# Kernel tuning notes

Hardware: AMD Instinct MI355X
Metric: run time of the kernel (lower is better)

## Reference

```python
import jax, jax.numpy as jnp
import numpy as np

NZ = 1024       # opts.nz (== NH so layer-0 input weights stack with other layers)
NH = 1024       # opts.nh
NSTATE = 64     # opts.n_state
NLAYERS = 4
MAX_PRIM_LEN = 100
T = MAX_PRIM_LEN + 1   # max_unroll=True runs exactly max_prim_len+1 steps
P_BIAS = 1.0           # opts.dec_p_bias


def setup_inputs() -> dict:
    key = jax.random.key(0)
    ks = jax.random.split(key, 9)
    s_ih = 1.0 / np.sqrt(NH)
    u = lambda k, shape: jax.random.uniform(k, shape, jnp.float32, -s_ih, s_ih)
    return {
        "z": jax.random.normal(ks[0], (1, NZ), jnp.float32),
        # torch LSTM params, gate order (i, f, g, o); layer0 input dim == NZ == NH
        "Wih": u(ks[1], (NLAYERS, 4 * NH, NH)),
        "Whh": u(ks[2], (NLAYERS, 4 * NH, NH)),
        "bih": u(ks[3], (NLAYERS, 4 * NH)),
        "bhh": u(ks[4], (NLAYERS, 4 * NH)),
        "Ws": u(ks[5], (NSTATE, NH)),
        "bs": u(ks[6], (NSTATE,)),
        "Wp": u(ks[7], (2, NH)),
        "bp": u(ks[8], (2,)),
    }


def reference(z, Wih, Whh, bih, bhh, Ws, bs, Wp, bp):
    z0 = z.reshape(-1)  # (NZ,)
    zeros = jnp.zeros_like(z0)

    def step(carry, i):
        h, c = carry                      # each (NLAYERS, NH)
        x = jnp.where(i == 0, z0, zeros)  # input is z at t=0, zeros after
        hs, cs = [], []
        inp = x
        for l in range(NLAYERS):
            gates = Wih[l] @ inp + bih[l] + Whh[l] @ h[l] + bhh[l]
            gi, gf, gg, go = jnp.split(gates, 4)
            cl = jax.nn.sigmoid(gf) * c[l] + jax.nn.sigmoid(gi) * jnp.tanh(gg)
            hl = jax.nn.sigmoid(go) * jnp.tanh(cl)
            hs.append(hl)
            cs.append(cl)
            inp = hl
        o = inp                            # top-layer output, (NH,)
        s = Ws @ o + bs                    # state head, (NSTATE,)
        logits = (Wp @ o + bp).at[0].add(P_BIAS)
        p = jax.nn.softmax(logits)         # (2,)
        last = i == T - 1                  # torch: t > max_prim_len -> force [0,1]
        p = jnp.where(last, jnp.array([0.0, 1.0], p.dtype), p)
        samp = jnp.where(last, 1, 0).astype(jnp.int64)  # max_unroll forces 0 until last
        return (jnp.stack(hs), jnp.stack(cs)), (s, p, samp)

    h0 = jnp.zeros((NLAYERS, NH), z.dtype)
    _, (states, probs, samples) = jax.lax.scan(step, (h0, h0), jnp.arange(T))
    return states[:, None, :], probs[:, None, :], samples[:, None]
```

## Files before the change

kernel.cpp:

```cpp
#include <hip/hip_runtime.h>


#define TT    101
#define NBLK  256
#define NTH   512
#define NREP  8
#define SLAB_U32 512
#define HB16_BYTES (4 * TT * NREP * SLAB_U32 * 4)
#define OUT_PROBS 6464
#define OUT_SAMP  6666
#define SENT 0xFFFFFFFFu

typedef _Float16 h2 __attribute__((ext_vector_type(2)));

__device__ __forceinline__ h2 mkh2(float a, float b) {
    h2 r; r.x = (_Float16)a; r.y = (_Float16)b; return r;
}
__device__ __forceinline__ unsigned pack2(float a, float b) {
    return __builtin_bit_cast(unsigned, mkh2(a, b));
}
__device__ __forceinline__ h2 as_h2(unsigned u) { return __builtin_bit_cast(h2, u); }

#if __has_builtin(__builtin_amdgcn_fdot2)
__device__ __forceinline__ float fdot2(h2 a, h2 b, float c) {
    return __builtin_amdgcn_fdot2(a, b, c, false);
}
#else
__device__ __forceinline__ float fdot2(h2 a, h2 b, float c) {
    return fmaf((float)a.x, (float)b.x, fmaf((float)a.y, (float)b.y, c));
}
#endif

__device__ __forceinline__ uint4 load16_bypass(const uint4* p) {
    uint4 r;
    asm volatile("global_load_dwordx4 %0, %1, off sc0 sc1\n\ts_waitcnt vmcnt(0)"
                 : "=v"(r) : "v"(p) : "memory");
    return r;
}
__device__ __forceinline__ void store4_bypass(unsigned* p, unsigned v) {
    asm volatile("global_store_dword %0, %1, off sc0 sc1" :: "v"(p), "v"(v) : "memory");
}
__device__ __forceinline__ uint4 poll16(const uint4* p) {
    uint4 r = load16_bypass(p);
    while (r.x == SENT || r.y == SENT || r.z == SENT || r.w == SENT) {
        __builtin_amdgcn_s_sleep(1);
        r = load16_bypass(p);
    }
    return r;
}

__device__ __forceinline__ float wave_sum(float x) {
    int v;
    v = __builtin_amdgcn_update_dpp(0, __builtin_bit_cast(int, x), 0x111, 0xf, 0xf, false);
    x += __builtin_bit_cast(float, v);
    v = __builtin_amdgcn_update_dpp(0, __builtin_bit_cast(int, x), 0x112, 0xf, 0xf, false);
    x += __builtin_bit_cast(float, v);
    v = __builtin_amdgcn_update_dpp(0, __builtin_bit_cast(int, x), 0x114, 0xf, 0xe, false);
    x += __builtin_bit_cast(float, v);
    v = __builtin_amdgcn_update_dpp(0, __builtin_bit_cast(int, x), 0x118, 0xf, 0xc, false);
    x += __builtin_bit_cast(float, v);
    v = __builtin_amdgcn_update_dpp(0, __builtin_bit_cast(int, x), 0x142, 0xa, 0xf, false);
    x += __builtin_bit_cast(float, v);
    v = __builtin_amdgcn_update_dpp(0, __builtin_bit_cast(int, x), 0x143, 0xc, 0xf, false);
    x += __builtin_bit_cast(float, v);
    return __builtin_bit_cast(float, __builtin_amdgcn_readlane(__builtin_bit_cast(int, x), 63));
}

__device__ __forceinline__ float sigm(float x) { return 1.f / (1.f + expf(-x)); }

__global__ __launch_bounds__(NTH, 2) void lstm_kernel(
    const float* __restrict__ z,
    const float* __restrict__ Wih, const float* __restrict__ Whh,
    const float* __restrict__ bih, const float* __restrict__ bhh,
    const float* __restrict__ Ws,  const float* __restrict__ bs,
    const float* __restrict__ Wp,  const float* __restrict__ bp,
    unsigned* __restrict__ hb16, float* __restrict__ out)
{
    const int tid  = threadIdx.x;
    const int wv   = tid >> 6;
    const int lane = tid & 63;
    const int l    = blockIdx.x >> 6;
    const int gb   = blockIdx.x & 63;
    const int uA   = (gb << 4) + (wv << 1);

    __shared__ __align__(16) uint4 vh4[256];
    __shared__ unsigned hout[8];

    h2 w[8][16];
    #pragma unroll
    for (int r = 0; r < 8; ++r) {
        const int u = uA + (r >> 2);
        const int g = r & 3;
        const size_t row = ((size_t)((l << 12) + (g << 10) + u)) << 10;
        const float4* pa = (const float4*)(Whh + row + (lane << 3));
        const float4* pb = (const float4*)(Whh + row + 512 + (lane << 3));
        const float4* pc = (const float4*)(Wih + row + (lane << 3));
        const float4* pd = (const float4*)(Wih + row + 512 + (lane << 3));
        float4 f;
        f = pa[0]; w[r][0]  = mkh2(f.x, f.y); w[r][1]  = mkh2(f.z, f.w);
        f = pa[1]; w[r][2]  = mkh2(f.x, f.y); w[r][3]  = mkh2(f.z, f.w);
        f = pb[0]; w[r][4]  = mkh2(f.x, f.y); w[r][5]  = mkh2(f.z, f.w);
        f = pb[1]; w[r][6]  = mkh2(f.x, f.y); w[r][7]  = mkh2(f.z, f.w);
        f = pc[0]; w[r][8]  = mkh2(f.x, f.y); w[r][9]  = mkh2(f.z, f.w);
        f = pc[1]; w[r][10] = mkh2(f.x, f.y); w[r][11] = mkh2(f.z, f.w);
        f = pd[0]; w[r][12] = mkh2(f.x, f.y); w[r][13] = mkh2(f.z, f.w);
        f = pd[1]; w[r][14] = mkh2(f.x, f.y); w[r][15] = mkh2(f.z, f.w);
    }

    float bA[4], bB[4];
    #pragma unroll
    for (int g = 0; g < 4; ++g) {
        const int iA = (l << 12) + (g << 10) + uA;
        bA[g] = bih[iA] + bhh[iA];
        bB[g] = bih[iA + 1] + bhh[iA + 1];
    }

    const bool role_states = (l == 0 && wv == 6);
    const bool role_probs  = (l == 1 && gb == 0 && wv == 6);
    float hw0[16], hw1[16], hb0 = 0.f, hb1 = 0.f;
    if (role_states) {
        #pragma unroll
        for (int k = 0; k < 16; ++k) hw0[k] = Ws[(gb << 10) + (lane << 4) + k];
        hb0 = bs[gb];
    } else if (role_probs) {
        #pragma unroll
        for (int k = 0; k < 16; ++k) {
            hw0[k] = Wp[(lane << 4) + k];
            hw1[k] = Wp[1024 + (lane << 4) + k];
        }
        hb0 = bp[0]; hb1 = bp[1];
    }
    int th = 0;

    float cstA = 0.f, cstB = 0.f;

    #pragma unroll 1
    for (int t = 0; t < TT; ++t) {
        const bool full = (l > 0) || (t == 0);
        const int rep = (gb + wv) & (NREP - 1);

        if (wv < 2) {
            const int c = (wv << 6) + lane;
            if (t == 0) vh4[c] = make_uint4(0, 0, 0, 0);
            else {
                const uint4* slab = (const uint4*)(hb16 + (size_t)((l * TT + t - 1) * NREP + rep) * SLAB_U32);
                vh4[c] = poll16(slab + c);
            }
        } else if (wv < 4) {
            const int c = ((wv - 2) << 6) + lane;
            if (l > 0) {
                const uint4* slab = (const uint4*)(hb16 + (size_t)(((l - 1) * TT + t) * NREP + rep) * SLAB_U32);
                vh4[128 + c] = poll16(slab + c);
            } else if (t == 0) {
                const float4 f0 = *(const float4*)(z + (c << 3));
                const float4 f1 = *(const float4*)(z + (c << 3) + 4);
                vh4[128 + c] = make_uint4(pack2(f0.x, f0.y), pack2(f0.z, f0.w),
                                          pack2(f1.x, f1.y), pack2(f1.z, f1.w));
            }
        }
        __syncthreads();

        float acc[8] = {0.f, 0.f, 0.f, 0.f, 0.f, 0.f, 0.f, 0.f};
        {
            const uint4 A1 = vh4[lane];
            const uint4 A2 = vh4[64 + lane];
            const unsigned a8[8] = {A1.x, A1.y, A1.z, A1.w, A2.x, A2.y, A2.z, A2.w};
            #pragma unroll
            for (int k = 0; k < 8; ++k) {
                const h2 v2 = as_h2(a8[k]);
                #pragma unroll
                for (int r = 0; r < 8; ++r) acc[r] = fdot2(w[r][k], v2, acc[r]);
            }
            if (full) {
                const uint4 B1 = vh4[128 + lane];
                const uint4 B2 = vh4[192 + lane];
                const unsigned b8[8] = {B1.x, B1.y, B1.z, B1.w, B2.x, B2.y, B2.z, B2.w};
                #pragma unroll
                for (int k = 0; k < 8; ++k) {
                    const h2 v2 = as_h2(b8[k]);
                    #pragma unroll
                    for (int r = 0; r < 8; ++r) acc[r] = fdot2(w[r][8 + k], v2, acc[r]);
                }
            }
        }

        float tot[8];
        #pragma unroll
        for (int r = 0; r < 8; ++r) tot[r] = wave_sum(acc[r]);

        cstA = fmaf(sigm(tot[1] + bA[1]), cstA, sigm(tot[0] + bA[0]) * tanhf(tot[2] + bA[2]));
        cstB = fmaf(sigm(tot[5] + bB[1]), cstB, sigm(tot[4] + bB[0]) * tanhf(tot[6] + bB[2]));
        const float hA = sigm(tot[3] + bA[3]) * tanhf(cstA);
        const float hB = sigm(tot[7] + bB[3]) * tanhf(cstB);
        if (lane == 0) hout[wv] = pack2(hA, hB);
        __syncthreads();

        if (wv == 7) {
            const unsigned val = hout[lane & 7];
            unsigned* addr = hb16 + (size_t)(l * TT + t) * NREP * SLAB_U32
                           + (size_t)(lane >> 3) * SLAB_U32 + (gb << 3) + (lane & 7);
            store4_bypass(addr, val);
        } else if ((role_states || role_probs) && th < TT && th <= t - 3) {
            const int hrep = (gb + th) & (NREP - 1);
            const uint4* slab3 = (const uint4*)(hb16 + (size_t)((3 * TT + th) * NREP + hrep) * SLAB_U32);
            const uint4 r0 = load16_bypass(slab3 + (lane << 1));
            const uint4 r1 = load16_bypass(slab3 + (lane << 1) + 1);
            const bool ok = !(r0.x == SENT || r0.y == SENT || r0.z == SENT || r0.w == SENT ||
                              r1.x == SENT || r1.y == SENT || r1.z == SENT || r1.w == SENT);
            if (__ballot(ok) == ~0ull) {
                const unsigned u8[8] = {r0.x, r0.y, r0.z, r0.w, r1.x, r1.y, r1.z, r1.w};
                if (role_states) {
                    float a = 0.f;
                    #pragma unroll
                    for (int j = 0; j < 8; ++j) {
                        const h2 p = as_h2(u8[j]);
                        a = fmaf(hw0[2 * j], (float)p.x, a);
                        a = fmaf(hw0[2 * j + 1], (float)p.y, a);
                    }
                    const float tots = wave_sum(a);
                    if (lane == 0) out[th * 64 + gb] = tots + hb0;
                } else {
                    float a0 = 0.f, a1 = 0.f;
                    #pragma unroll
                    for (int j = 0; j < 8; ++j) {
                        const h2 p = as_h2(u8[j]);
                        a0 = fmaf(hw0[2 * j], (float)p.x, a0); a0 = fmaf(hw0[2 * j + 1], (float)p.y, a0);
                        a1 = fmaf(hw1[2 * j], (float)p.x, a1); a1 = fmaf(hw1[2 * j + 1], (float)p.y, a1);
                    }
                    const float t0 = wave_sum(a0), t1 = wave_sum(a1);
                    if (lane == 0) {
                        float p0, p1;
                        if (th == TT - 1) { p0 = 0.f; p1 = 1.f; }
                        else {
                            const float l0 = t0 + hb0 + 1.0f;
                            const float l1 = t1 + hb1;
                            const float m  = fmaxf(l0, l1);
                            const float e0 = expf(l0 - m), e1 = expf(l1 - m);
                            const float inv = 1.f / (e0 + e1);
                            p0 = e0 * inv; p1 = e1 * inv;
                        }
                        out[OUT_PROBS + 2 * th]     = p0;
                        out[OUT_PROBS + 2 * th + 1] = p1;
                        out[OUT_SAMP + th] = (th == TT - 1) ? 1.0f : 0.0f;
                    }
                }
                ++th;
            }
        }
    }

    if (role_states || role_probs) {
        while (th < TT) {
            const int hrep = (gb + th) & (NREP - 1);
            const uint4* slab3 = (const uint4*)(hb16 + (size_t)((3 * TT + th) * NREP + hrep) * SLAB_U32);
            const uint4 r0 = poll16(slab3 + (lane << 1));
            const uint4 r1 = poll16(slab3 + (lane << 1) + 1);
            const unsigned u8[8] = {r0.x, r0.y, r0.z, r0.w, r1.x, r1.y, r1.z, r1.w};
            if (role_states) {
                float a = 0.f;
                #pragma unroll
                for (int j = 0; j < 8; ++j) {
                    const h2 p = as_h2(u8[j]);
                    a = fmaf(hw0[2 * j], (float)p.x, a);
                    a = fmaf(hw0[2 * j + 1], (float)p.y, a);
                }
                const float tots = wave_sum(a);
                if (lane == 0) out[th * 64 + gb] = tots + hb0;
            } else {
                float a0 = 0.f, a1 = 0.f;
                #pragma unroll
                for (int j = 0; j < 8; ++j) {
                    const h2 p = as_h2(u8[j]);
                    a0 = fmaf(hw0[2 * j], (float)p.x, a0); a0 = fmaf(hw0[2 * j + 1], (float)p.y, a0);
                    a1 = fmaf(hw1[2 * j], (float)p.x, a1); a1 = fmaf(hw1[2 * j + 1], (float)p.y, a1);
                }
                const float t0 = wave_sum(a0), t1 = wave_sum(a1);
                if (lane == 0) {
                    float p0, p1;
                    if (th == TT - 1) { p0 = 0.f; p1 = 1.f; }
                    else {
                        const float l0 = t0 + hb0 + 1.0f;
                        const float l1 = t1 + hb1;
                        const float m  = fmaxf(l0, l1);
                        const float e0 = expf(l0 - m), e1 = expf(l1 - m);
                        const float inv = 1.f / (e0 + e1);
                        p0 = e0 * inv; p1 = e1 * inv;
                    }
                    out[OUT_PROBS + 2 * th]     = p0;
                    out[OUT_PROBS + 2 * th + 1] = p1;
                    out[OUT_SAMP + th] = (th == TT - 1) ? 1.0f : 0.0f;
                }
            }
            ++th;
        }
    }
}

extern "C" void kernel_launch(void* const* d_in, const int* in_sizes, int n_in,
                              void* d_out, int out_size, void* d_ws, size_t ws_size,
                              hipStream_t stream)
{
    const float* z   = (const float*)d_in[0];
    const float* Wih = (const float*)d_in[1];
    const float* Whh = (const float*)d_in[2];
    const float* bih = (const float*)d_in[3];
    const float* bhh = (const float*)d_in[4];
    const float* Ws  = (const float*)d_in[5];
    const float* bs  = (const float*)d_in[6];
    const float* Wp  = (const float*)d_in[7];
    const float* bp  = (const float*)d_in[8];
    float* out = (float*)d_out;

    unsigned* hb16 = (unsigned*)d_ws;

    hipMemsetAsync(hb16, 0xFF, HB16_BYTES, stream);
    lstm_kernel<<<NBLK, NTH, 0, stream>>>(z, Wih, Whh, bih, bhh,
                                          Ws, bs, Wp, bp, hb16, out);
}
```

Baseline: 506.2 us.

## Replace pre-publish block barrier with LDS flag handoff, fast activations, paired loads

The per-step __syncthreads before publishing h is replaced by a sentinel-flagged LDS slot that wave 7 spins on, so the publishing wave can store the new hidden state as soon as all eight waves have written. The barrier moves to the end of the step. Sigmoid and tanh now use __expf-based fast approximations, and the two head-polling loads are issued together before a single wait. This shortens the serial critical path of each recurrent step, at the cost of LDS spin-waiting and slightly lower activation accuracy.

```diff
diff --git a/kernel.cpp b/kernel.cpp
--- a/kernel.cpp
+++ b/kernel.cpp
@@ -40,6 +40,13 @@
 __device__ __forceinline__ void store4_bypass(unsigned* p, unsigned v) {
     asm volatile("global_store_dword %0, %1, off sc0 sc1" :: "v"(p), "v"(v) : "memory");
 }
+__device__ __forceinline__ void load32_bypass2(const uint4* p0, const uint4* p1,
+                                               uint4& r0, uint4& r1) {
+    asm volatile("global_load_dwordx4 %0, %2, off sc0 sc1\n\t"
+                 "global_load_dwordx4 %1, %3, off sc0 sc1\n\t"
+                 "s_waitcnt vmcnt(0)"
+                 : "=&v"(r0), "=&v"(r1) : "v"(p0), "v"(p1) : "memory");
+}
 __device__ __forceinline__ uint4 poll16(const uint4* p) {
     uint4 r = load16_bypass(p);
     while (r.x == SENT || r.y == SENT || r.z == SENT || r.w == SENT) {
@@ -48,6 +55,9 @@
     }
     return r;
 }
+__device__ __forceinline__ bool stale(const uint4& u) {
+    return (u.x == SENT) | (u.y == SENT) | (u.z == SENT) | (u.w == SENT);
+}
 
 __device__ __forceinline__ float wave_sum(float x) {
     int v;
@@ -66,7 +76,8 @@
     return __builtin_bit_cast(float, __builtin_amdgcn_readlane(__builtin_bit_cast(int, x), 63));
 }
 
-__device__ __forceinline__ float sigm(float x) { return 1.f / (1.f + expf(-x)); }
+__device__ __forceinline__ float sigm(float x)   { return 1.f / (1.f + __expf(-x)); }
+__device__ __forceinline__ float tanh_f(float x) { return 1.f - 2.f / (1.f + __expf(x + x)); }
 
 __global__ __launch_bounds__(NTH, 2) void lstm_kernel(
     const float* __restrict__ z,
@@ -134,6 +145,8 @@
 
     float cstA = 0.f, cstB = 0.f;
 
+    if (tid < 8) hout[tid] = SENT;
+
     #pragma unroll 1
     for (int t = 0; t < TT; ++t) {
         const bool full = (l > 0) || (t == 0);
@@ -188,25 +201,26 @@
         #pragma unroll
         for (int r = 0; r < 8; ++r) tot[r] = wave_sum(acc[r]);
 
-        cstA = fmaf(sigm(tot[1] + bA[1]), cstA, sigm(tot[0] + bA[0]) * tanhf(tot[2] + bA[2]));
-        cstB = fmaf(sigm(tot[5] + bB[1]), cstB, sigm(tot[4] + bB[0]) * tanhf(tot[6] + bB[2]));
-        const float hA = sigm(tot[3] + bA[3]) * tanhf(cstA);
-        const float hB = sigm(tot[7] + bB[3]) * tanhf(cstB);
-        if (lane == 0) hout[wv] = pack2(hA, hB);
-        __syncthreads();
+        cstA = fmaf(sigm(tot[1] + bA[1]), cstA, sigm(tot[0] + bA[0]) * tanh_f(tot[2] + bA[2]));
+        cstB = fmaf(sigm(tot[5] + bB[1]), cstB, sigm(tot[4] + bB[0]) * tanh_f(tot[6] + bB[2]));
+        const float hA = sigm(tot[3] + bA[3]) * tanh_f(cstA);
+        const float hB = sigm(tot[7] + bB[3]) * tanh_f(cstB);
+        if (lane == 0) ((volatile unsigned*)hout)[wv] = pack2(hA, hB);
 
         if (wv == 7) {
-            const unsigned val = hout[lane & 7];
+            volatile unsigned* vho = (volatile unsigned*)hout;
+            unsigned v = vho[lane & 7];
+            while (v == SENT) { v = vho[lane & 7]; }
             unsigned* addr = hb16 + (size_t)(l * TT + t) * NREP * SLAB_U32
                            + (size_t)(lane >> 3) * SLAB_U32 + (gb << 3) + (lane & 7);
-            store4_bypass(addr, val);
+            store4_bypass(addr, v);
+            if (lane < 8) vho[lane] = SENT;
         } else if ((role_states || role_probs) && th < TT && th <= t - 3) {
             const int hrep = (gb + th) & (NREP - 1);
             const uint4* slab3 = (const uint4*)(hb16 + (size_t)((3 * TT + th) * NREP + hrep) * SLAB_U32);
-            const uint4 r0 = load16_bypass(slab3 + (lane << 1));
-            const uint4 r1 = load16_bypass(slab3 + (lane << 1) + 1);
-            const bool ok = !(r0.x == SENT || r0.y == SENT || r0.z == SENT || r0.w == SENT ||
-                              r1.x == SENT || r1.y == SENT || r1.z == SENT || r1.w == SENT);
+            uint4 r0, r1;
+            load32_bypass2(slab3 + (lane << 1), slab3 + (lane << 1) + 1, r0, r1);
+            const bool ok = !(stale(r0) | stale(r1));
             if (__ballot(ok) == ~0ull) {
                 const unsigned u8[8] = {r0.x, r0.y, r0.z, r0.w, r1.x, r1.y, r1.z, r1.w};
                 if (role_states) {
@@ -247,14 +261,19 @@
                 ++th;
             }
         }
+        __syncthreads();
     }
 
     if (role_states || role_probs) {
         while (th < TT) {
             const int hrep = (gb + th) & (NREP - 1);
             const uint4* slab3 = (const uint4*)(hb16 + (size_t)((3 * TT + th) * NREP + hrep) * SLAB_U32);
-            const uint4 r0 = poll16(slab3 + (lane << 1));
-            const uint4 r1 = poll16(slab3 + (lane << 1) + 1);
+            uint4 r0, r1;
+            for (;;) {
+                load32_bypass2(slab3 + (lane << 1), slab3 + (lane << 1) + 1, r0, r1);
+                if (!(stale(r0) | stale(r1))) break;
+                __builtin_amdgcn_s_sleep(1);
+            }
             const unsigned u8[8] = {r0.x, r0.y, r0.z, r0.w, r1.x, r1.y, r1.z, r1.w};
             if (role_states) {
                 float a = 0.f;
```

New measurement: 460.4 us (median of 2 runs). 9.1% less time.
